# Optimization experiments

Hardware: AMD Instinct MI355X
Metric: run time of the kernel (lower is better)

Reference implementation:

```python
import jax, jax.numpy as jnp
import numpy as np

B, L, H, HEADS = 4, 256, 256, 4
D = H // HEADS
NEG = jnp.float32(-2.0**32 + 1)


def setup_inputs() -> dict:
    key = jax.random.key(0)
    ks = jax.random.split(key, 16)
    inp = {
        "queries": jax.random.normal(ks[0], (B, L, H), jnp.float32),
        "keys": jax.random.normal(ks[1], (B, L, H), jnp.float32),
        "values": jax.random.normal(ks[2], (B, L, H), jnp.float32),
        "time_matrix_K": jax.random.normal(ks[3], (B, L, L, H), jnp.float32),
        "time_matrix_V": jax.random.normal(ks[4], (B, L, L, H), jnp.float32),
        "abs_pos_K": jax.random.normal(ks[5], (B, L, H), jnp.float32),
        "abs_pos_V": jax.random.normal(ks[6], (B, L, H), jnp.float32),
        "time_mask": jax.random.randint(ks[7], (B, L), 0, 2) == 1,
        "future_time_mask": jnp.triu(jnp.ones((L, L), bool), k=1),
        # linear layer params (torch Linear: y = x @ W.T + b)
        "Wq": jax.random.normal(ks[8], (H, H), jnp.float32) / np.sqrt(H),
        "bq": jax.random.normal(ks[9], (H,), jnp.float32) * 0.01,
        "Wk": jax.random.normal(ks[10], (H, H), jnp.float32) / np.sqrt(H),
        "bk": jax.random.normal(ks[11], (H,), jnp.float32) * 0.01,
        "Wv": jax.random.normal(ks[12], (H, H), jnp.float32) / np.sqrt(H),
        "bv": jax.random.normal(ks[13], (H,), jnp.float32) * 0.01,
    }
    return inp


def _split_heads(x):  # [B,L,H] -> [h,B,L,d]
    b, l, _ = x.shape
    return x.reshape(b, l, HEADS, D).transpose(2, 0, 1, 3)


def _split_heads_rel(t):  # [B,L,L,H] -> [h,B,L,L,d]
    b, l, _, _ = t.shape
    return t.reshape(b, l, l, HEADS, D).transpose(3, 0, 1, 2, 4)


def reference(queries, keys, values, time_matrix_K, time_matrix_V,
              abs_pos_K, abs_pos_V, time_mask, future_time_mask,
              Wq, bq, Wk, bk, Wv, bv):
    Q = _split_heads(queries @ Wq.T + bq)   # [h,B,L,d]
    K = _split_heads(keys @ Wk.T + bk)
    V = _split_heads(values @ Wv.T + bv)
    tK = _split_heads_rel(time_matrix_K)    # [h,B,L,L,d]
    tV = _split_heads_rel(time_matrix_V)
    pK = _split_heads(abs_pos_K)            # [h,B,L,d]
    pV = _split_heads(abs_pos_V)

    scores = jnp.einsum("hbqd,hbkd->hbqk", Q, K)
    scores += jnp.einsum("hbqd,hbkd->hbqk", Q, pK)
    scores += jnp.einsum("hbqkd,hbqd->hbqk", tK, Q)
    scores = scores / jnp.sqrt(jnp.float32(D))

    mask = time_mask[None, :, :, None] | future_time_mask[None, None, :, :]
    scores = jnp.where(mask, NEG, scores)
    attn = jax.nn.softmax(scores, axis=-1)  # [h,B,L,L]  (dropout: eval mode)

    out = jnp.einsum("hbqk,hbkd->hbqd", attn, V)
    out += jnp.einsum("hbqk,hbkd->hbqd", attn, pV)
    out += jnp.einsum("hbqk,hbqkd->hbqd", attn, tV)
    # merge heads: [h,B,L,d] -> [B,L,H]
    return out.transpose(1, 2, 0, 3).reshape(B, L, H)
```

## Files before the change

kernel.cpp:

```cpp
#include <hip/hip_runtime.h>
#include <math.h>
#include <stdint.h>

#define LSEQ 256
#define HD 256

typedef float floatx4 __attribute__((ext_vector_type(4)));

__device__ __forceinline__ float dot4(float4 a, float4 b) {
    return a.x * b.x + a.y * b.y + a.z * b.z + a.w * b.w;
}
__device__ __forceinline__ float4 add4(float4 a, float4 b) {
    return make_float4(a.x + b.x, a.y + b.y, a.z + b.z, a.w + b.w);
}
__device__ __forceinline__ float4 ldnt4(const float* p) {
    floatx4 r = __builtin_nontemporal_load((const floatx4*)p);
    return make_float4(r.x, r.y, r.z, r.w);
}

__global__ __launch_bounds__(256) void proj_kernel(
    const float* __restrict__ queries, const float* __restrict__ keys,
    const float* __restrict__ values,
    const float* __restrict__ apK, const float* __restrict__ apV,
    const float* __restrict__ Wq, const float* __restrict__ bq,
    const float* __restrict__ Wk, const float* __restrict__ bk,
    const float* __restrict__ Wv, const float* __restrict__ bv,
    float* __restrict__ Qo, float* __restrict__ Ko, float* __restrict__ Vo)
{
    const int R = 4;
    int tid = threadIdx.x;
    int row0 = blockIdx.x * R;

    float aq[R] = {0.f, 0.f, 0.f, 0.f};
    float ak[R] = {0.f, 0.f, 0.f, 0.f};
    float av[R] = {0.f, 0.f, 0.f, 0.f};

    const float* wq = Wq + tid * HD;
    const float* wk = Wk + tid * HD;
    const float* wv = Wv + tid * HD;

    #pragma unroll 2
    for (int i = 0; i < HD; i += 4) {
        float4 wq4 = *(const float4*)(wq + i);
        float4 wk4 = *(const float4*)(wk + i);
        float4 wv4 = *(const float4*)(wv + i);
        #pragma unroll
        for (int r = 0; r < R; ++r) {
            float4 xq = *(const float4*)(queries + (row0 + r) * HD + i);
            float4 xk = *(const float4*)(keys    + (row0 + r) * HD + i);
            float4 xv = *(const float4*)(values  + (row0 + r) * HD + i);
            aq[r] += dot4(xq, wq4);
            ak[r] += dot4(xk, wk4);
            av[r] += dot4(xv, wv4);
        }
    }
    #pragma unroll
    for (int r = 0; r < R; ++r) {
        int idx = (row0 + r) * HD + tid;
        Qo[idx] = aq[r] + bq[tid];
        Ko[idx] = ak[r] + bk[tid] + apK[idx];
        Vo[idx] = av[r] + bv[tid] + apV[idx];
    }
}

__global__ __launch_bounds__(256) void scores_kernel(
    const float* __restrict__ Q, const float* __restrict__ Keff,
    const float* __restrict__ tK, const int* __restrict__ tmask,
    float* __restrict__ sc_out)
{
    int bid = blockIdx.x;
    int bq = bid >> 2;
    int c = bid & 3;
    int q = bq & 255;
    int b = bq >> 8;
    int k0c = c << 6;
    if (k0c > q || tmask[bq]) return;

    int tid = threadIdx.x;
    int v = tid >> 6;
    int lane = tid & 63;
    int head = lane >> 4;
    int le4 = lane * 4;

    const float* tKr = tK + (size_t)bq * (LSEQ * HD);
    const float* Kb  = Keff + b * (LSEQ * HD);
    float4 q4 = *(const float4*)(Q + bq * HD + le4);
    float* scrow = sc_out + (size_t)(bq * 4 + head) * LSEQ;

    int r0 = k0c + v * 16;
    int rend = min(r0 + 16, q + 1);

    int k = r0;
    for (; k + 3 < rend; k += 4) {
        float4 t0 = ldnt4(tKr + (k    ) * HD + le4);
        float4 t1 = ldnt4(tKr + (k + 1) * HD + le4);
        float4 t2 = ldnt4(tKr + (k + 2) * HD + le4);
        float4 t3 = ldnt4(tKr + (k + 3) * HD + le4);
        float4 c0 = *(const float4*)(Kb + (k    ) * HD + le4);
        float4 c1 = *(const float4*)(Kb + (k + 1) * HD + le4);
        float4 c2 = *(const float4*)(Kb + (k + 2) * HD + le4);
        float4 c3 = *(const float4*)(Kb + (k + 3) * HD + le4);
        float s0 = dot4(q4, add4(t0, c0));
        float s1 = dot4(q4, add4(t1, c1));
        float s2 = dot4(q4, add4(t2, c2));
        float s3 = dot4(q4, add4(t3, c3));
        #pragma unroll
        for (int off = 1; off <= 8; off <<= 1) {
            s0 += __shfl_xor(s0, off);
            s1 += __shfl_xor(s1, off);
            s2 += __shfl_xor(s2, off);
            s3 += __shfl_xor(s3, off);
        }
        if ((lane & 15) == 0)
            *(float4*)(scrow + k) = make_float4(s0 * 0.125f, s1 * 0.125f,
                                                s2 * 0.125f, s3 * 0.125f);
    }
    for (; k < rend; ++k) {
        float4 t0 = ldnt4(tKr + k * HD + le4);
        float4 c0 = *(const float4*)(Kb + k * HD + le4);
        float s0 = dot4(q4, add4(t0, c0));
        #pragma unroll
        for (int off = 1; off <= 8; off <<= 1)
            s0 += __shfl_xor(s0, off);
        if ((lane & 15) == 0) scrow[k] = s0 * 0.125f;
    }
}

__global__ __launch_bounds__(256) void softmax_kernel(
    float* __restrict__ sc, const int* __restrict__ tmask)
{
    int bq = blockIdx.x;
    if (tmask[bq]) return;
    int q = bq & 255;
    int tid = threadIdx.x;
    int w = tid >> 6;
    int lane = tid & 63;
    float* row = sc + (size_t)(bq * 4 + w) * LSEQ;
    int k0 = lane * 4;
    float4 vv = *(const float4*)(row + k0);
    float x0 = (k0 + 0 <= q) ? vv.x : -INFINITY;
    float x1 = (k0 + 1 <= q) ? vv.y : -INFINITY;
    float x2 = (k0 + 2 <= q) ? vv.z : -INFINITY;
    float x3 = (k0 + 3 <= q) ? vv.w : -INFINITY;
    float m = fmaxf(fmaxf(x0, x1), fmaxf(x2, x3));
    #pragma unroll
    for (int off = 32; off >= 1; off >>= 1)
        m = fmaxf(m, __shfl_xor(m, off));
    float e0 = __expf(x0 - m);
    float e1 = __expf(x1 - m);
    float e2 = __expf(x2 - m);
    float e3 = __expf(x3 - m);
    float ssum = e0 + e1 + e2 + e3;
    #pragma unroll
    for (int off = 32; off >= 1; off >>= 1)
        ssum += __shfl_xor(ssum, off);
    float inv = 1.0f / ssum;
    *(float4*)(row + k0) = make_float4(e0 * inv, e1 * inv, e2 * inv, e3 * inv);
}

__global__ __launch_bounds__(256) void pv_kernel(
    const float* __restrict__ Veff, const float* __restrict__ tV,
    const float* __restrict__ attn, const int* __restrict__ tmask,
    float* __restrict__ part)
{
    __shared__ float outp[4][256];

    int bid = blockIdx.x;
    int bq = bid >> 2;
    int c = bid & 3;
    int q = bq & 255;
    int b = bq >> 8;
    bool masked = tmask[bq] != 0;
    int kstart = c << 6;
    if (!masked && kstart > q) return;
    int kendc = min(kstart + 64, masked ? LSEQ : q + 1);

    int tid = threadIdx.x;
    int v = tid >> 6;
    int lane = tid & 63;
    int head = lane >> 4;
    int le4 = lane * 4;

    const float* tVr = tV + (size_t)bq * (LSEQ * HD);
    const float* Vb  = Veff + b * (LSEQ * HD);
    const float* arow = attn + (size_t)(bq * 4 + head) * LSEQ;
    const float uw = 1.0f / 256.0f;

    int r0 = kstart + v * 16;
    int rend = min(r0 + 16, kendc);

    float4 acc = make_float4(0.f, 0.f, 0.f, 0.f);
    int k = r0;
    for (; k + 3 < rend; k += 4) {
        float4 t0 = ldnt4(tVr + (k    ) * HD + le4);
        float4 t1 = ldnt4(tVr + (k + 1) * HD + le4);
        float4 t2 = ldnt4(tVr + (k + 2) * HD + le4);
        float4 t3 = ldnt4(tVr + (k + 3) * HD + le4);
        float4 v0 = *(const float4*)(Vb + (k    ) * HD + le4);
        float4 v1 = *(const float4*)(Vb + (k + 1) * HD + le4);
        float4 v2 = *(const float4*)(Vb + (k + 2) * HD + le4);
        float4 v3 = *(const float4*)(Vb + (k + 3) * HD + le4);
        float4 a4;
        if (masked) a4 = make_float4(uw, uw, uw, uw);
        else        a4 = *(const float4*)(arow + k);
        acc.x += a4.x * (t0.x + v0.x) + a4.y * (t1.x + v1.x)
               + a4.z * (t2.x + v2.x) + a4.w * (t3.x + v3.x);
        acc.y += a4.x * (t0.y + v0.y) + a4.y * (t1.y + v1.y)
               + a4.z * (t2.y + v2.y) + a4.w * (t3.y + v3.y);
        acc.z += a4.x * (t0.z + v0.z) + a4.y * (t1.z + v1.z)
               + a4.z * (t2.z + v2.z) + a4.w * (t3.z + v3.z);
        acc.w += a4.x * (t0.w + v0.w) + a4.y * (t1.w + v1.w)
               + a4.z * (t2.w + v2.w) + a4.w * (t3.w + v3.w);
    }
    for (; k < rend; ++k) {
        float4 t0 = ldnt4(tVr + k * HD + le4);
        float4 v0 = *(const float4*)(Vb + k * HD + le4);
        float a0 = masked ? uw : arow[k];
        acc.x += a0 * (t0.x + v0.x);
        acc.y += a0 * (t0.y + v0.y);
        acc.z += a0 * (t0.z + v0.z);
        acc.w += a0 * (t0.w + v0.w);
    }
    *(float4*)(&outp[v][le4]) = acc;
    __syncthreads();
    float o = outp[0][tid] + outp[1][tid] + outp[2][tid] + outp[3][tid];
    part[((size_t)((c << 10) | bq)) * HD + tid] = o;
}

__global__ __launch_bounds__(256) void reduce_kernel(
    const float* __restrict__ part, const int* __restrict__ tmask,
    float* __restrict__ out)
{
    int bq = blockIdx.x;
    int q = bq & 255;
    int tid = threadIdx.x;
    int nch = tmask[bq] ? 4 : ((q >> 6) + 1);
    float o = 0.f;
    for (int c = 0; c < nch; ++c)
        o += part[((size_t)((c << 10) | bq)) * HD + tid];
    out[(size_t)bq * HD + tid] = o;
}

extern "C" void kernel_launch(void* const* d_in, const int* in_sizes, int n_in,
                              void* d_out, int out_size, void* d_ws, size_t ws_size,
                              hipStream_t stream) {
    const float* queries = (const float*)d_in[0];
    const float* keys    = (const float*)d_in[1];
    const float* values  = (const float*)d_in[2];
    const float* tK      = (const float*)d_in[3];
    const float* tV      = (const float*)d_in[4];
    const float* apK     = (const float*)d_in[5];
    const float* apV     = (const float*)d_in[6];
    const int*   tmask   = (const int*)d_in[7];
    const float* Wq = (const float*)d_in[9];
    const float* bq = (const float*)d_in[10];
    const float* Wk = (const float*)d_in[11];
    const float* bk = (const float*)d_in[12];
    const float* Wv = (const float*)d_in[13];
    const float* bv = (const float*)d_in[14];

    float* ws = (float*)d_ws;
    float* Qo     = ws;
    float* Ko     = ws + 262144;
    float* Vo     = ws + 524288;
    float* scores = ws + 786432;
    float* partb  = ws + 1835008;
    float* out = (float*)d_out;

    proj_kernel<<<256, 256, 0, stream>>>(queries, keys, values, apK, apV,
                                         Wq, bq, Wk, bk, Wv, bv, Qo, Ko, Vo);
    scores_kernel<<<4096, 256, 0, stream>>>(Qo, Ko, tK, tmask, scores);
    softmax_kernel<<<1024, 256, 0, stream>>>(scores, tmask);
    pv_kernel<<<4096, 256, 0, stream>>>(Vo, tV, scores, tmask, partb);
    reduce_kernel<<<1024, 256, 0, stream>>>(partb, tmask, out);
}
```

Before: 108.6 us.

## Fuse scores with softmax and PV with reduction using one 512-thread block per row

Merges the score and softmax kernels into one block per query row that keeps scores in shared memory. It also merges the PV and reduce kernels into one block per row using 8 warps, which removes the partial-sum buffer and two launches. Masked rows precompute the mean of V once and only sum tV. Nontemporal loads are replaced with plain loads. The cost is fewer, larger blocks, which may lower parallelism for short causal rows.

Measured after the change: 137.7 us. 1.27x slower.

```diff
diff --git a/kernel.cpp b/kernel.cpp
--- a/kernel.cpp
+++ b/kernel.cpp
@@ -5,17 +5,11 @@
 #define LSEQ 256
 #define HD 256
 
-typedef float floatx4 __attribute__((ext_vector_type(4)));
-
 __device__ __forceinline__ float dot4(float4 a, float4 b) {
     return a.x * b.x + a.y * b.y + a.z * b.z + a.w * b.w;
 }
 __device__ __forceinline__ float4 add4(float4 a, float4 b) {
     return make_float4(a.x + b.x, a.y + b.y, a.z + b.z, a.w + b.w);
-}
-__device__ __forceinline__ float4 ldnt4(const float* p) {
-    floatx4 r = __builtin_nontemporal_load((const floatx4*)p);
-    return make_float4(r.x, r.y, r.z, r.w);
 }
 
 __global__ __launch_bounds__(256) void proj_kernel(
@@ -63,21 +57,33 @@
     }
 }
 
-__global__ __launch_bounds__(256) void scores_kernel(
+__global__ __launch_bounds__(256) void vmean_kernel(
+    const float* __restrict__ Veff, float* __restrict__ Vm)
+{
+    int b = blockIdx.x;
+    int t = threadIdx.x;
+    const float* Vb = Veff + b * (LSEQ * HD);
+    float s = 0.f;
+    #pragma unroll 4
+    for (int k = 0; k < LSEQ; ++k)
+        s += Vb[k * HD + t];
+    Vm[b * HD + t] = s * (1.0f / 256.0f);
+}
+
+__global__ __launch_bounds__(512) void scoresmax_kernel(
     const float* __restrict__ Q, const float* __restrict__ Keff,
     const float* __restrict__ tK, const int* __restrict__ tmask,
-    float* __restrict__ sc_out)
-{
-    int bid = blockIdx.x;
-    int bq = bid >> 2;
-    int c = bid & 3;
+    float* __restrict__ att)
+{
+    __shared__ float sc[4][260];
+
+    int bq = blockIdx.x;
     int q = bq & 255;
     int b = bq >> 8;
-    int k0c = c << 6;
-    if (k0c > q || tmask[bq]) return;
+    if (tmask[bq]) return;
 
     int tid = threadIdx.x;
-    int v = tid >> 6;
+    int w = tid >> 6;
     int lane = tid & 63;
     int head = lane >> 4;
     int le4 = lane * 4;
@@ -85,17 +91,18 @@
     const float* tKr = tK + (size_t)bq * (LSEQ * HD);
     const float* Kb  = Keff + b * (LSEQ * HD);
     float4 q4 = *(const float4*)(Q + bq * HD + le4);
-    float* scrow = sc_out + (size_t)(bq * 4 + head) * LSEQ;
-
-    int r0 = k0c + v * 16;
-    int rend = min(r0 + 16, q + 1);
+
+    int nk = q + 1;
+    int run = (nk + 7) >> 3;
+    int r0 = w * run;
+    int rend = min(r0 + run, nk);
 
     int k = r0;
     for (; k + 3 < rend; k += 4) {
-        float4 t0 = ldnt4(tKr + (k    ) * HD + le4);
-        float4 t1 = ldnt4(tKr + (k + 1) * HD + le4);
-        float4 t2 = ldnt4(tKr + (k + 2) * HD + le4);
-        float4 t3 = ldnt4(tKr + (k + 3) * HD + le4);
+        float4 t0 = *(const float4*)(tKr + (k    ) * HD + le4);
+        float4 t1 = *(const float4*)(tKr + (k + 1) * HD + le4);
+        float4 t2 = *(const float4*)(tKr + (k + 2) * HD + le4);
+        float4 t3 = *(const float4*)(tKr + (k + 3) * HD + le4);
         float4 c0 = *(const float4*)(Kb + (k    ) * HD + le4);
         float4 c1 = *(const float4*)(Kb + (k + 1) * HD + le4);
         float4 c2 = *(const float4*)(Kb + (k + 2) * HD + le4);
@@ -111,134 +118,136 @@
             s2 += __shfl_xor(s2, off);
             s3 += __shfl_xor(s3, off);
         }
-        if ((lane & 15) == 0)
-            *(float4*)(scrow + k) = make_float4(s0 * 0.125f, s1 * 0.125f,
-                                                s2 * 0.125f, s3 * 0.125f);
+        if ((lane & 15) == 0) {
+            sc[head][k    ] = s0 * 0.125f;
+            sc[head][k + 1] = s1 * 0.125f;
+            sc[head][k + 2] = s2 * 0.125f;
+            sc[head][k + 3] = s3 * 0.125f;
+        }
     }
     for (; k < rend; ++k) {
-        float4 t0 = ldnt4(tKr + k * HD + le4);
+        float4 t0 = *(const float4*)(tKr + k * HD + le4);
         float4 c0 = *(const float4*)(Kb + k * HD + le4);
         float s0 = dot4(q4, add4(t0, c0));
         #pragma unroll
         for (int off = 1; off <= 8; off <<= 1)
             s0 += __shfl_xor(s0, off);
-        if ((lane & 15) == 0) scrow[k] = s0 * 0.125f;
-    }
-}
-
-__global__ __launch_bounds__(256) void softmax_kernel(
-    float* __restrict__ sc, const int* __restrict__ tmask)
-{
+        if ((lane & 15) == 0) sc[head][k] = s0 * 0.125f;
+    }
+    __syncthreads();
+
+    if (w < 4) {
+        int k0 = lane * 4;
+        float4 vv = *(const float4*)(&sc[w][k0]);
+        float x0 = (k0 + 0 <= q) ? vv.x : -INFINITY;
+        float x1 = (k0 + 1 <= q) ? vv.y : -INFINITY;
+        float x2 = (k0 + 2 <= q) ? vv.z : -INFINITY;
+        float x3 = (k0 + 3 <= q) ? vv.w : -INFINITY;
+        float m = fmaxf(fmaxf(x0, x1), fmaxf(x2, x3));
+        #pragma unroll
+        for (int off = 32; off >= 1; off >>= 1)
+            m = fmaxf(m, __shfl_xor(m, off));
+        float e0 = __expf(x0 - m);
+        float e1 = __expf(x1 - m);
+        float e2 = __expf(x2 - m);
+        float e3 = __expf(x3 - m);
+        float ssum = e0 + e1 + e2 + e3;
+        #pragma unroll
+        for (int off = 32; off >= 1; off >>= 1)
+            ssum += __shfl_xor(ssum, off);
+        float inv = 1.0f / ssum;
+        *(float4*)(att + (size_t)(bq * 4 + w) * LSEQ + k0) =
+            make_float4(e0 * inv, e1 * inv, e2 * inv, e3 * inv);
+    }
+}
+
+__global__ __launch_bounds__(512) void pv_kernel(
+    const float* __restrict__ Veff, const float* __restrict__ tV,
+    const float* __restrict__ att, const float* __restrict__ Vm,
+    const int* __restrict__ tmask, float* __restrict__ out)
+{
+    __shared__ float outp[8][256];
+
     int bq = blockIdx.x;
-    if (tmask[bq]) return;
     int q = bq & 255;
+    int b = bq >> 8;
+    bool masked = tmask[bq] != 0;
+
     int tid = threadIdx.x;
     int w = tid >> 6;
     int lane = tid & 63;
-    float* row = sc + (size_t)(bq * 4 + w) * LSEQ;
-    int k0 = lane * 4;
-    float4 vv = *(const float4*)(row + k0);
-    float x0 = (k0 + 0 <= q) ? vv.x : -INFINITY;
-    float x1 = (k0 + 1 <= q) ? vv.y : -INFINITY;
-    float x2 = (k0 + 2 <= q) ? vv.z : -INFINITY;
-    float x3 = (k0 + 3 <= q) ? vv.w : -INFINITY;
-    float m = fmaxf(fmaxf(x0, x1), fmaxf(x2, x3));
-    #pragma unroll
-    for (int off = 32; off >= 1; off >>= 1)
-        m = fmaxf(m, __shfl_xor(m, off));
-    float e0 = __expf(x0 - m);
-    float e1 = __expf(x1 - m);
-    float e2 = __expf(x2 - m);
-    float e3 = __expf(x3 - m);
-    float ssum = e0 + e1 + e2 + e3;
-    #pragma unroll
-    for (int off = 32; off >= 1; off >>= 1)
-        ssum += __shfl_xor(ssum, off);
-    float inv = 1.0f / ssum;
-    *(float4*)(row + k0) = make_float4(e0 * inv, e1 * inv, e2 * inv, e3 * inv);
-}
-
-__global__ __launch_bounds__(256) void pv_kernel(
-    const float* __restrict__ Veff, const float* __restrict__ tV,
-    const float* __restrict__ attn, const int* __restrict__ tmask,
-    float* __restrict__ part)
-{
-    __shared__ float outp[4][256];
-
-    int bid = blockIdx.x;
-    int bq = bid >> 2;
-    int c = bid & 3;
-    int q = bq & 255;
-    int b = bq >> 8;
-    bool masked = tmask[bq] != 0;
-    int kstart = c << 6;
-    if (!masked && kstart > q) return;
-    int kendc = min(kstart + 64, masked ? LSEQ : q + 1);
-
-    int tid = threadIdx.x;
-    int v = tid >> 6;
-    int lane = tid & 63;
     int head = lane >> 4;
     int le4 = lane * 4;
 
     const float* tVr = tV + (size_t)bq * (LSEQ * HD);
-    const float* Vb  = Veff + b * (LSEQ * HD);
-    const float* arow = attn + (size_t)(bq * 4 + head) * LSEQ;
-    const float uw = 1.0f / 256.0f;
-
-    int r0 = kstart + v * 16;
-    int rend = min(r0 + 16, kendc);
+
+    int nk = masked ? LSEQ : (q + 1);
+    int run = (nk + 7) >> 3;
+    int r0 = w * run;
+    int rend = min(r0 + run, nk);
 
     float4 acc = make_float4(0.f, 0.f, 0.f, 0.f);
-    int k = r0;
-    for (; k + 3 < rend; k += 4) {
-        float4 t0 = ldnt4(tVr + (k    ) * HD + le4);
-        float4 t1 = ldnt4(tVr + (k + 1) * HD + le4);
-        float4 t2 = ldnt4(tVr + (k + 2) * HD + le4);
-        float4 t3 = ldnt4(tVr + (k + 3) * HD + le4);
-        float4 v0 = *(const float4*)(Vb + (k    ) * HD + le4);
-        float4 v1 = *(const float4*)(Vb + (k + 1) * HD + le4);
-        float4 v2 = *(const float4*)(Vb + (k + 2) * HD + le4);
-        float4 v3 = *(const float4*)(Vb + (k + 3) * HD + le4);
-        float4 a4;
-        if (masked) a4 = make_float4(uw, uw, uw, uw);
-        else        a4 = *(const float4*)(arow + k);
-        acc.x += a4.x * (t0.x + v0.x) + a4.y * (t1.x + v1.x)
-               + a4.z * (t2.x + v2.x) + a4.w * (t3.x + v3.x);
-        acc.y += a4.x * (t0.y + v0.y) + a4.y * (t1.y + v1.y)
-               + a4.z * (t2.y + v2.y) + a4.w * (t3.y + v3.y);
-        acc.z += a4.x * (t0.z + v0.z) + a4.y * (t1.z + v1.z)
-               + a4.z * (t2.z + v2.z) + a4.w * (t3.z + v3.z);
-        acc.w += a4.x * (t0.w + v0.w) + a4.y * (t1.w + v1.w)
-               + a4.z * (t2.w + v2.w) + a4.w * (t3.w + v3.w);
-    }
-    for (; k < rend; ++k) {
-        float4 t0 = ldnt4(tVr + k * HD + le4);
-        float4 v0 = *(const float4*)(Vb + k * HD + le4);
-        float a0 = masked ? uw : arow[k];
-        acc.x += a0 * (t0.x + v0.x);
-        acc.y += a0 * (t0.y + v0.y);
-        acc.z += a0 * (t0.z + v0.z);
-        acc.w += a0 * (t0.w + v0.w);
-    }
-    *(float4*)(&outp[v][le4]) = acc;
+    if (masked) {
+        int k = r0;
+        for (; k + 3 < rend; k += 4) {
+            float4 t0 = *(const float4*)(tVr + (k    ) * HD + le4);
+            float4 t1 = *(const float4*)(tVr + (k + 1) * HD + le4);
+            float4 t2 = *(const float4*)(tVr + (k + 2) * HD + le4);
+            float4 t3 = *(const float4*)(tVr + (k + 3) * HD + le4);
+            acc.x += (t0.x + t1.x) + (t2.x + t3.x);
+            acc.y += (t0.y + t1.y) + (t2.y + t3.y);
+            acc.z += (t0.z + t1.z) + (t2.z + t3.z);
+            acc.w += (t0.w + t1.w) + (t2.w + t3.w);
+        }
+        for (; k < rend; ++k) {
+            float4 t0 = *(const float4*)(tVr + k * HD + le4);
+            acc.x += t0.x; acc.y += t0.y; acc.z += t0.z; acc.w += t0.w;
+        }
+    } else {
+        const float* Vb = Veff + b * (LSEQ * HD);
+        const float* arow = att + (size_t)(bq * 4 + head) * LSEQ;
+        int k = r0;
+        for (; k + 3 < rend; k += 4) {
+            float4 t0 = *(const float4*)(tVr + (k    ) * HD + le4);
+            float4 t1 = *(const float4*)(tVr + (k + 1) * HD + le4);
+            float4 t2 = *(const float4*)(tVr + (k + 2) * HD + le4);
+            float4 t3 = *(const float4*)(tVr + (k + 3) * HD + le4);
+            float4 v0 = *(const float4*)(Vb + (k    ) * HD + le4);
+            float4 v1 = *(const float4*)(Vb + (k + 1) * HD + le4);
+            float4 v2 = *(const float4*)(Vb + (k + 2) * HD + le4);
+            float4 v3 = *(const float4*)(Vb + (k + 3) * HD + le4);
+            float a0 = arow[k    ];
+            float a1 = arow[k + 1];
+            float a2 = arow[k + 2];
+            float a3 = arow[k + 3];
+            acc.x += a0 * (t0.x + v0.x) + a1 * (t1.x + v1.x)
+                   + a2 * (t2.x + v2.x) + a3 * (t3.x + v3.x);
+            acc.y += a0 * (t0.y + v0.y) + a1 * (t1.y + v1.y)
+                   + a2 * (t2.y + v2.y) + a3 * (t3.y + v3.y);
+            acc.z += a0 * (t0.z + v0.z) + a1 * (t1.z + v1.z)
+                   + a2 * (t2.z + v2.z) + a3 * (t3.z + v3.z);
+            acc.w += a0 * (t0.w + v0.w) + a1 * (t1.w + v1.w)
+                   + a2 * (t2.w + v2.w) + a3 * (t3.w + v3.w);
+        }
+        for (; k < rend; ++k) {
+            float4 t0 = *(const float4*)(tVr + k * HD + le4);
+            float4 v0 = *(const float4*)(Vb + k * HD + le4);
+            float a0 = arow[k];
+            acc.x += a0 * (t0.x + v0.x);
+            acc.y += a0 * (t0.y + v0.y);
+            acc.z += a0 * (t0.z + v0.z);
+            acc.w += a0 * (t0.w + v0.w);
+        }
+    }
+    *(float4*)(&outp[w][le4]) = acc;
     __syncthreads();
-    float o = outp[0][tid] + outp[1][tid] + outp[2][tid] + outp[3][tid];
-    part[((size_t)((c << 10) | bq)) * HD + tid] = o;
-}
-
-__global__ __launch_bounds__(256) void reduce_kernel(
-    const float* __restrict__ part, const int* __restrict__ tmask,
-    float* __restrict__ out)
-{
-    int bq = blockIdx.x;
-    int q = bq & 255;
-    int tid = threadIdx.x;
-    int nch = tmask[bq] ? 4 : ((q >> 6) + 1);
-    float o = 0.f;
-    for (int c = 0; c < nch; ++c)
-        o += part[((size_t)((c << 10) | bq)) * HD + tid];
-    out[(size_t)bq * HD + tid] = o;
+    if (tid < 256) {
+        float o = 0.f;
+        #pragma unroll
+        for (int p = 0; p < 8; ++p) o += outp[p][tid];
+        if (masked) o = o * (1.0f / 256.0f) + Vm[b * HD + tid];
+        out[(size_t)bq * HD + tid] = o;
+    }
 }
 
 extern "C" void kernel_launch(void* const* d_in, const int* in_sizes, int n_in,
@@ -260,17 +269,16 @@
     const float* bv = (const float*)d_in[14];
 
     float* ws = (float*)d_ws;
-    float* Qo     = ws;
-    float* Ko     = ws + 262144;
-    float* Vo     = ws + 524288;
-    float* scores = ws + 786432;
-    float* partb  = ws + 1835008;
+    float* Qo  = ws;
+    float* Ko  = ws + 262144;
+    float* Vo  = ws + 524288;
+    float* att = ws + 786432;
+    float* Vm  = ws + 1835008;
     float* out = (float*)d_out;
 
     proj_kernel<<<256, 256, 0, stream>>>(queries, keys, values, apK, apV,
                                          Wq, bq, Wk, bk, Wv, bv, Qo, Ko, Vo);
-    scores_kernel<<<4096, 256, 0, stream>>>(Qo, Ko, tK, tmask, scores);
-    softmax_kernel<<<1024, 256, 0, stream>>>(scores, tmask);
-    pv_kernel<<<4096, 256, 0, stream>>>(Vo, tV, scores, tmask, partb);
-    reduce_kernel<<<1024, 256, 0, stream>>>(partb, tmask, out);
-}
+    vmean_kernel<<<4, 256, 0, stream>>>(Vo, Vm);
+    scoresmax_kernel<<<1024, 512, 0, stream>>>(Qo, Ko, tK, tmask, att);
+    pv_kernel<<<1024, 512, 0, stream>>>(Vo, tV, att, Vm, tmask, out);
+}
```
